# Kernel optimization log

Measured on AMD Instinct MI355X. Metric: run time of the kernel, lower is better.

## Reference

```python
import jax, jax.numpy as jnp
import numpy as np

N = 100000   # nodes
E = 3200000  # edges
D = 128      # input feature dim (lazy in_channels of gat1)
H = 1        # heads
C1, C2 = 16, 32
NEG_SLOPE = 0.2


def setup_inputs() -> dict:
    key = jax.random.key(0)
    ks = jax.random.split(key, 20)
    g = lambda k, shape, s=0.05: (jax.random.normal(k, shape, dtype=jnp.float32) * s)
    return {
        "x": jax.random.normal(ks[0], (N, D), dtype=jnp.float32),
        "edges": jax.random.randint(ks[1], (2, E), 0, N, dtype=jnp.int32),
        "edge_weights": jax.random.uniform(ks[2], (E, 1), dtype=jnp.float32),
        # GATv2 layer 1 (in=D, out=16, heads=1, edge_dim=1)
        "Wl1": g(ks[3], (D, H * C1)), "bl1": jnp.zeros((H * C1,), jnp.float32),
        "Wr1": g(ks[4], (D, H * C1)), "br1": jnp.zeros((H * C1,), jnp.float32),
        "We1": g(ks[5], (1, H * C1)),
        "att1": g(ks[6], (H, C1)),
        "b1": jnp.zeros((C1,), jnp.float32),
        # GATv2 layer 2 (in=16, out=32, heads=1, edge_dim=1)
        "Wl2": g(ks[7], (C1, H * C2)), "bl2": jnp.zeros((H * C2,), jnp.float32),
        "Wr2": g(ks[8], (C1, H * C2)), "br2": jnp.zeros((H * C2,), jnp.float32),
        "We2": g(ks[9], (1, H * C2)),
        "att2": g(ks[10], (H, C2)),
        "b2": jnp.zeros((C2,), jnp.float32),
    }


def _segment_softmax(e, seg, num_segments):
    # numerically-stable softmax over edges grouped by destination node
    m = jax.ops.segment_max(e, seg, num_segments=num_segments)  # [N,H]
    ex = jnp.exp(e - m[seg])
    s = jax.ops.segment_sum(ex, seg, num_segments=num_segments)  # [N,H]
    return ex / (s[seg] + 1e-16)


def _gatv2(x, src, dst, edge_attr, Wl, bl, Wr, br, We, att, b, num_nodes, heads, out_ch):
    xl = (x @ Wl + bl).reshape(-1, heads, out_ch)          # [N,H,C] source transform
    xr = (x @ Wr + br).reshape(-1, heads, out_ch)          # [N,H,C] target transform
    xe = (edge_attr @ We).reshape(-1, heads, out_ch)       # [E,H,C] edge transform
    s = jax.nn.leaky_relu(xl[src] + xr[dst] + xe, NEG_SLOPE)  # [E,H,C]
    e = jnp.einsum('ehc,hc->eh', s, att)                   # [E,H] scores
    alpha = _segment_softmax(e, dst, num_nodes)            # [E,H]
    out = jax.ops.segment_sum(alpha[..., None] * xl[src], dst, num_segments=num_nodes)
    out = out.mean(axis=1) + b                             # concat=False -> mean over heads
    return out, alpha


def reference(x, edges, edge_weights, Wl1, bl1, Wr1, br1, We1, att1, b1,
              Wl2, bl2, Wr2, br2, We2, att2, b2):
    src, dst = edges[0], edges[1]
    h, alpha1 = _gatv2(x, src, dst, edge_weights, Wl1, bl1, Wr1, br1, We1, att1, b1, N, H, C1)
    h = jax.nn.relu(h)
    # layer-1 attention coefficients become layer-2 edge features ([E, heads=1])
    _, alpha2 = _gatv2(h, src, dst, alpha1, Wl2, bl2, Wr2, br2, We2, att2, b2, N, H, C2)
    return edges, alpha2
```

## Files before the change

### kernel.cpp

```cpp
#include <hip/hip_runtime.h>
#include <hip/hip_bf16.h>


#define NN 100000
#define EE 3200000
#define DD 128
#define CC1 16
#define CC2 32
#define NEG_SLOPE 0.2f

#define NPB  128
#define NBK  782
#define BCAP 5120
#define ACH  4096
#define ABLK 782

typedef __hip_bfloat16 bf16;

__device__ __forceinline__ float b2f(bf16 v) { return __bfloat162float(v); }

__device__ __forceinline__ void ld8bf(const bf16* p, float* f) {
    uint4 u = *(const uint4*)p;
    const unsigned w[4] = {u.x, u.y, u.z, u.w};
#pragma unroll
    for (int i = 0; i < 4; i++) {
        f[2 * i]     = __uint_as_float(w[i] << 16);
        f[2 * i + 1] = __uint_as_float(w[i] & 0xffff0000u);
    }
}

__device__ __forceinline__ unsigned enc_f(float x) {
    unsigned b = __float_as_uint(x);
    return (b & 0x80000000u) ? ~b : (b | 0x80000000u);
}
__device__ __forceinline__ float dec_f(unsigned u) {
    unsigned b = (u & 0x80000000u) ? (u & 0x7fffffffu) : ~u;
    return __uint_as_float(b);
}

__global__ void lin1_kernel(const float* __restrict__ x,
                            const float* __restrict__ Wl, const float* __restrict__ bl,
                            const float* __restrict__ Wr, const float* __restrict__ br,
                            bf16* __restrict__ xl1, bf16* __restrict__ xr1) {
    __shared__ float Ws[DD][32];
    __shared__ float xs[8][DD];
    const int t = threadIdx.x;
    for (int i = t; i < DD * CC1; i += 256) {
        int k = i >> 4, c = i & 15;
        Ws[k][c]      = Wl[i];
        Ws[k][c + 16] = Wr[i];
    }
    const int node0 = blockIdx.x * 8;
    for (int i = t; i < 8 * DD; i += 256) {
        int n = i >> 7, k = i & 127;
        xs[n][k] = x[(node0 + n) * DD + k];
    }
    __syncthreads();
    const int n = t >> 5, c = t & 31;
    const int node = node0 + n;
    float acc = 0.f;
#pragma unroll 16
    for (int k = 0; k < DD; k++) acc += xs[n][k] * Ws[k][c];
    if (c < 16) xl1[node * CC1 + c]        = __float2bfloat16(acc + bl[c]);
    else        xr1[node * CC1 + (c - 16)] = __float2bfloat16(acc + br[c - 16]);
}

__global__ void edge1bin_kernel(const int* __restrict__ edges,
                                const float* __restrict__ ew,
                                const bf16* __restrict__ xl1, const bf16* __restrict__ xr1,
                                const float* __restrict__ We1, const float* __restrict__ att1,
                                float* __restrict__ e1,
                                uint2* __restrict__ tmp, int* __restrict__ gcur) {
    __shared__ float Wes[CC1], atts[CC1];
    __shared__ int cnts[NBK], gbase[NBK], lfill[NBK];
    const int t = threadIdx.x;
    if (t < CC1) { Wes[t] = We1[t]; atts[t] = att1[t]; }
    for (int b = t; b < NBK; b += 256) { cnts[b] = 0; lfill[b] = 0; }
    __syncthreads();
    const int base = blockIdx.x * ACH;
    unsigned pk[16]; float ev[16]; int bk[16];
#pragma unroll
    for (int k = 0; k < 16; k++) {
        const int i = base + k * 256 + t;
        bk[k] = -1;
        if (i < EE) {
            const int s = edges[i], d = edges[EE + i];
            const float w = ew[i];
            float a[CC1], b[CC1];
            ld8bf(xl1 + s * CC1, a); ld8bf(xl1 + s * CC1 + 8, a + 8);
            ld8bf(xr1 + d * CC1, b); ld8bf(xr1 + d * CC1 + 8, b + 8);
            float acc = 0.f;
#pragma unroll
            for (int c = 0; c < CC1; c++) {
                float v = a[c] + b[c] + w * Wes[c];
                v = v > 0.f ? v : NEG_SLOPE * v;
                acc += v * atts[c];
            }
            e1[i] = acc;
            bk[k] = d >> 7;
            pk[k] = (unsigned)(d & 127) | ((unsigned)s << 7);
            ev[k] = acc;
            atomicAdd(&cnts[bk[k]], 1);
        }
    }
    __syncthreads();
    for (int b = t; b < NBK; b += 256)
        if (cnts[b] > 0) gbase[b] = atomicAdd(&gcur[b], cnts[b]);
    __syncthreads();
#pragma unroll
    for (int k = 0; k < 16; k++) {
        if (bk[k] >= 0) {
            const int slot = gbase[bk[k]] + atomicAdd(&lfill[bk[k]], 1);
            tmp[(size_t)bk[k] * BCAP + slot] = make_uint2(pk[k], __float_as_uint(ev[k]));
        }
    }
}

__global__ void scanB_kernel(const int* __restrict__ gcur, int* __restrict__ bbase,
                             int* __restrict__ off) {
    __shared__ int part[1024];
    const int t = threadIdx.x;
    part[t] = (t < NBK) ? gcur[t] : 0;
    __syncthreads();
    for (int o = 1; o < 1024; o <<= 1) {
        int v = (t >= o) ? part[t - o] : 0;
        __syncthreads();
        part[t] += v;
        __syncthreads();
    }
    if (t < NBK) bbase[t] = part[t] - gcur[t];
    if (t == 0) off[NN] = EE;
}

__global__ void binB2_kernel(const uint2* __restrict__ tmp, const int* __restrict__ gcur,
                             const int* __restrict__ bbase,
                             uint2* __restrict__ csr2, int* __restrict__ off) {
    __shared__ int cnt[NPB];
    __shared__ int loff[NPB];
    const int t = threadIdx.x;
    const int b = blockIdx.x;
    const int count = gcur[b];
    const uint2* rec = tmp + (size_t)b * BCAP;
    for (int i = t; i < NPB; i += 512) cnt[i] = 0;
    __syncthreads();
    for (int j = t; j < count; j += 512) atomicAdd(&cnt[rec[j].x & 127u], 1);
    __syncthreads();
    if (t == 0) {
        int run = 0;
#pragma unroll
        for (int i = 0; i < NPB; i++) { loff[i] = run; run += cnt[i]; }
    }
    __syncthreads();
    const int base = bbase[b];
    const int n0 = b * NPB;
    for (int i = t; i < NPB; i += 512) {
        const int node = n0 + i;
        if (node < NN) off[node] = base + loff[i];
    }
    for (int j = t; j < count; j += 512) {
        const uint2 r = rec[j];
        const int d = (int)(r.x & 127u);
        const int rr = atomicSub(&cnt[d], 1);
        const int pos = base + loff[d] + rr - 1;
        const float p = __expf(__uint_as_float(r.y));
        csr2[pos] = make_uint2(r.x >> 7, __float_as_uint(p));
    }
}

__global__ void node1f_kernel(const int* __restrict__ off, const uint2* __restrict__ csr2,
                              const bf16* __restrict__ xl1,
                              float* __restrict__ den1, bf16* __restrict__ out1) {
    const int t = blockIdx.x * 256 + threadIdx.x;
    const int n = t >> 4, c = t & 15;
    const int beg = off[n], end = off[n + 1];
    float l = 0.f, acc = 0.f;
    for (int j = beg; j < end; j++) {
        const uint2 r = csr2[j];
        const float p = __uint_as_float(r.y);
        acc += p * b2f(xl1[r.x * CC1 + c]);
        l += p;
    }
    out1[n * CC1 + c] = __float2bfloat16(l > 0.f ? acc / l : 0.f);
    if (c == 0) den1[n] = l;
}

__global__ void lin2_kernel(const bf16* __restrict__ out1, const float* __restrict__ b1,
                            const float* __restrict__ Wl2, const float* __restrict__ bl2,
                            const float* __restrict__ Wr2, const float* __restrict__ br2,
                            bf16* __restrict__ xl2, bf16* __restrict__ xr2) {
    __shared__ float Ws[CC1][64];
    __shared__ float hs[4][CC1];
    const int t = threadIdx.x;
    for (int i = t; i < CC1 * CC2; i += 256) {
        int k = i >> 5, c = i & 31;
        Ws[k][c]      = Wl2[i];
        Ws[k][c + 32] = Wr2[i];
    }
    const int node0 = blockIdx.x * 4;
    if (t < 64) {
        int n = t >> 4, k = t & 15;
        float v = b2f(out1[(node0 + n) * CC1 + k]) + b1[k];
        hs[n][k] = v > 0.f ? v : 0.f;
    }
    __syncthreads();
    const int n = t >> 6, c = t & 63;
    const int node = node0 + n;
    float acc = 0.f;
#pragma unroll
    for (int k = 0; k < CC1; k++) acc += hs[n][k] * Ws[k][c];
    if (c < 32) xl2[node * CC2 + c]        = __float2bfloat16(acc + bl2[c]);
    else        xr2[node * CC2 + (c - 32)] = __float2bfloat16(acc + br2[c - 32]);
}

__global__ void edge2bin_kernel(const int* __restrict__ edges,
                                float* __restrict__ e,
                                const float* __restrict__ den1,
                                const bf16* __restrict__ xl2, const bf16* __restrict__ xr2,
                                const float* __restrict__ We2, const float* __restrict__ att2,
                                uint2* __restrict__ tmp, int* __restrict__ gcur) {
    __shared__ float Wes[CC2], atts[CC2];
    __shared__ int cnts[NBK], gbase[NBK], lfill[NBK];
    const int t = threadIdx.x;
    if (t < CC2) { Wes[t] = We2[t]; atts[t] = att2[t]; }
    for (int b = t; b < NBK; b += 256) { cnts[b] = 0; lfill[b] = 0; }
    __syncthreads();
    const int base = blockIdx.x * ACH;
    unsigned pk[16]; float ev[16]; int bk[16];
#pragma unroll
    for (int k = 0; k < 16; k++) {
        const int i = base + k * 256 + t;
        bk[k] = -1;
        if (i < EE) {
            const int s = edges[i], d = edges[EE + i];
            const float w = __expf(e[i]) / (den1[d] + 1e-16f);
            float a[CC2], b[CC2];
#pragma unroll
            for (int q = 0; q < 4; q++) {
                ld8bf(xl2 + s * CC2 + 8 * q, a + 8 * q);
                ld8bf(xr2 + d * CC2 + 8 * q, b + 8 * q);
            }
            float acc = 0.f;
#pragma unroll
            for (int c = 0; c < CC2; c++) {
                float v = a[c] + b[c] + w * Wes[c];
                v = v > 0.f ? v : NEG_SLOPE * v;
                acc += v * atts[c];
            }
            e[i] = acc;
            bk[k] = d >> 7;
            pk[k] = (unsigned)(d & 127);
            ev[k] = acc;
            atomicAdd(&cnts[bk[k]], 1);
        }
    }
    __syncthreads();
    for (int b = t; b < NBK; b += 256)
        if (cnts[b] > 0) gbase[b] = atomicAdd(&gcur[b], cnts[b]);
    __syncthreads();
#pragma unroll
    for (int k = 0; k < 16; k++) {
        if (bk[k] >= 0) {
            const int slot = gbase[bk[k]] + atomicAdd(&lfill[bk[k]], 1);
            tmp[(size_t)bk[k] * BCAP + slot] = make_uint2(pk[k], __float_as_uint(ev[k]));
        }
    }
}

__global__ void nodeB2_kernel(const uint2* __restrict__ tmp, const int* __restrict__ gcur,
                              float* __restrict__ den2) {
    __shared__ float den[NPB];
    const int t = threadIdx.x;
    const int b = blockIdx.x;
    const int count = gcur[b];
    const uint2* rec = tmp + (size_t)b * BCAP;
    for (int i = t; i < NPB; i += 512) den[i] = 0.f;
    __syncthreads();
    for (int j = t; j < count; j += 512) {
        const uint2 r = rec[j];
        atomicAdd(&den[r.x & 127u], __expf(__uint_as_float(r.y)));
    }
    __syncthreads();
    const int n0 = b * NPB;
    for (int i = t; i < NPB; i += 512) {
        const int node = n0 + i;
        if (node < NN) den2[node] = den[i];
    }
}

__global__ void final2_kernel(const int* __restrict__ dst,
                              const float* __restrict__ e,
                              const float* __restrict__ den2,
                              float* __restrict__ out) {
    const int i = blockIdx.x * 256 + threadIdx.x;
    const int d = dst[i];
    out[2 * EE + i] = __expf(e[i]) / (den2[d] + 1e-16f);
}

__global__ void edges_kernel(const int* __restrict__ edges, float* __restrict__ out) {
    const int i = blockIdx.x * 256 + threadIdx.x;
    out[i] = (float)edges[i];
}

__global__ void edge1f_kernel(const int* __restrict__ edges,
                              const float* __restrict__ ew,
                              const bf16* __restrict__ xl1, const bf16* __restrict__ xr1,
                              const float* __restrict__ We1, const float* __restrict__ att1,
                              float* __restrict__ e1, int* __restrict__ cnt,
                              unsigned* __restrict__ m1enc) {
    __shared__ float Wes[CC1], atts[CC1];
    if (threadIdx.x < CC1) {
        Wes[threadIdx.x]  = We1[threadIdx.x];
        atts[threadIdx.x] = att1[threadIdx.x];
    }
    __syncthreads();
    const int e = blockIdx.x * 256 + threadIdx.x;
    const int s = edges[e], d = edges[EE + e];
    const float w = ew[e];
    float a[CC1], b[CC1];
    ld8bf(xl1 + s * CC1, a); ld8bf(xl1 + s * CC1 + 8, a + 8);
    ld8bf(xr1 + d * CC1, b); ld8bf(xr1 + d * CC1 + 8, b + 8);
    float acc = 0.f;
#pragma unroll
    for (int c = 0; c < CC1; c++) {
        float v = a[c] + b[c] + w * Wes[c];
        v = v > 0.f ? v : NEG_SLOPE * v;
        acc += v * atts[c];
    }
    e1[e] = acc;
    atomicAdd(&cnt[d], 1);
    atomicMax(&m1enc[d], enc_f(acc));
}

__global__ void scan_kernel(const int* __restrict__ cnt, int* __restrict__ off) {
    __shared__ int part[1024];
    const int t = threadIdx.x;
    const int chunk = (NN + 1023) / 1024;
    const int beg = t * chunk;
    const int end = min(beg + chunk, NN);
    int s = 0;
    for (int i = beg; i < end; i++) s += cnt[i];
    part[t] = s;
    __syncthreads();
    for (int o = 1; o < 1024; o <<= 1) {
        int v = (t >= o) ? part[t - o] : 0;
        __syncthreads();
        part[t] += v;
        __syncthreads();
    }
    int run = (t > 0) ? part[t - 1] : 0;
    for (int i = beg; i < end; i++) { off[i] = run; run += cnt[i]; }
    if (t == 1023) off[NN] = part[1023];
}

__global__ void scatter_kernel(const int* __restrict__ edges,
                               const int* __restrict__ off, int* __restrict__ cnt,
                               int* __restrict__ csr) {
    const int i = blockIdx.x * 256 + threadIdx.x;
    const int d = edges[EE + i];
    const int r = atomicSub(&cnt[d], 1);
    csr[off[d] + r - 1] = i;
}

__global__ void node1s_kernel(const int* __restrict__ off, const int* __restrict__ csr,
                              const int* __restrict__ edges,
                              const float* __restrict__ e1, const bf16* __restrict__ xl1,
                              float* __restrict__ den1, bf16* __restrict__ out1) {
    const int t = blockIdx.x * 256 + threadIdx.x;
    const int n = t >> 4, c = t & 15;
    const int beg = off[n], end = off[n + 1];
    float m = -3.0e38f, l = 0.f, acc = 0.f;
    for (int j = beg; j < end; j++) {
        const int eid = csr[j];
        const float s = e1[eid];
        const int src = edges[eid];
        const float xv = b2f(xl1[src * CC1 + c]);
        if (s > m) { const float r = __expf(m - s); l *= r; acc *= r; m = s; }
        const float p = __expf(s - m);
        l += p; acc += p * xv;
    }
    out1[n * CC1 + c] = __float2bfloat16(l > 0.f ? acc / l : 0.f);
    if (c == 0) den1[n] = l;
}

__global__ void edge2enc_kernel(const int* __restrict__ edges,
                                float* __restrict__ e,
                                const unsigned* __restrict__ m1enc,
                                const float* __restrict__ den1,
                                const bf16* __restrict__ xl2, const bf16* __restrict__ xr2,
                                const float* __restrict__ We2, const float* __restrict__ att2) {
    __shared__ float Wes[CC2], atts[CC2];
    if (threadIdx.x < CC2) {
        Wes[threadIdx.x]  = We2[threadIdx.x];
        atts[threadIdx.x] = att2[threadIdx.x];
    }
    __syncthreads();
    const int i = blockIdx.x * 256 + threadIdx.x;
    const int s = edges[i], d = edges[EE + i];
    const float w = __expf(e[i] - dec_f(m1enc[d])) / (den1[d] + 1e-16f);
    float a[CC2], b[CC2];
#pragma unroll
    for (int q = 0; q < 4; q++) {
        ld8bf(xl2 + s * CC2 + 8 * q, a + 8 * q);
        ld8bf(xr2 + d * CC2 + 8 * q, b + 8 * q);
    }
    float acc = 0.f;
#pragma unroll
    for (int c = 0; c < CC2; c++) {
        float v = a[c] + b[c] + w * Wes[c];
        v = v > 0.f ? v : NEG_SLOPE * v;
        acc += v * atts[c];
    }
    e[i] = acc;
}

__global__ void max2_kernel(const int* __restrict__ dst, const float* __restrict__ e2,
                            unsigned* __restrict__ m2) {
    const int i = blockIdx.x * 256 + threadIdx.x;
    atomicMax(&m2[dst[i]], enc_f(e2[i]));
}

__global__ void num2_kernel(const int* __restrict__ dst,
                            const unsigned* __restrict__ m2,
                            float* __restrict__ e, float* __restrict__ den2) {
    const int i = blockIdx.x * 256 + threadIdx.x;
    const int d = dst[i];
    const float v = __expf(e[i] - dec_f(m2[d]));
    e[i] = v;
    atomicAdd(&den2[d], v);
}

__global__ void finalold_kernel(const int* __restrict__ dst,
                                const float* __restrict__ e,
                                const float* __restrict__ den2,
                                float* __restrict__ out) {
    const int i = blockIdx.x * 256 + threadIdx.x;
    const int d = dst[i];
    out[2 * EE + i] = e[i] / (den2[d] + 1e-16f);
}

extern "C" void kernel_launch(void* const* d_in, const int* in_sizes, int n_in,
                              void* d_out, int out_size, void* d_ws, size_t ws_size,
                              hipStream_t stream) {
    const float* x    = (const float*)d_in[0];
    const int*  edges = (const int*)d_in[1];
    const float* ew   = (const float*)d_in[2];
    const float* Wl1  = (const float*)d_in[3];
    const float* bl1  = (const float*)d_in[4];
    const float* Wr1  = (const float*)d_in[5];
    const float* br1  = (const float*)d_in[6];
    const float* We1  = (const float*)d_in[7];
    const float* att1 = (const float*)d_in[8];
    const float* b1   = (const float*)d_in[9];
    const float* Wl2  = (const float*)d_in[10];
    const float* bl2  = (const float*)d_in[11];
    const float* Wr2  = (const float*)d_in[12];
    const float* br2  = (const float*)d_in[13];
    const float* We2  = (const float*)d_in[14];
    const float* att2 = (const float*)d_in[15];
    float* out = (float*)d_out;

    const int* dst = edges + EE;
    const int EG = EE / 256;

    const size_t dpBytes = (size_t)NBK * BCAP * 8;
    uint2* tmp   = (uint2*)d_ws;
    int*   gcur  = (int*)((char*)d_ws + dpBytes);
    int*   bbase = (int*)((char*)d_ws + dpBytes + 4096);
    uint2* csr2  = (uint2*)((char*)d_ws + dpBytes + 8192);
    int*   off   = (int*)((char*)d_ws + dpBytes + 8192 + (size_t)EE * 8);
    const size_t ws_need = dpBytes + 8192 + (size_t)EE * 8
                         + (size_t)(NN + 4) * 4;
    const bool fast = (d_ws != nullptr) && (ws_size >= ws_need);

    if (fast) {
        float* e = out;
        bf16*  xl2  = (bf16*)(out + EE);
        bf16*  xr2  = xl2 + NN * CC2;
        float* den2 = out + EE;
        float* den1 = out + 2 * EE;
        bf16*  xl1  = (bf16*)(den1 + NN);
        bf16*  xr1  = xl1 + NN * CC1;
        bf16*  out1 = xr1 + NN * CC1;

        hipMemsetAsync(gcur, 0, (size_t)NBK * sizeof(int), stream);
        lin1_kernel    <<<NN / 8, 256, 0, stream>>>(x, Wl1, bl1, Wr1, br1, xl1, xr1);
        edge1bin_kernel<<<ABLK, 256, 0, stream>>>(edges, ew, xl1, xr1, We1, att1,
                                                  e, tmp, gcur);
        scanB_kernel   <<<1, 1024, 0, stream>>>(gcur, bbase, off);
        binB2_kernel   <<<NBK, 512, 0, stream>>>(tmp, gcur, bbase, csr2, off);
        node1f_kernel  <<<NN * 16 / 256, 256, 0, stream>>>(off, csr2, xl1, den1, out1);
        lin2_kernel    <<<NN / 4, 256, 0, stream>>>(out1, b1, Wl2, bl2, Wr2, br2, xl2, xr2);
        hipMemsetAsync(gcur, 0, (size_t)NBK * sizeof(int), stream);
        edge2bin_kernel<<<ABLK, 256, 0, stream>>>(edges, e, den1, xl2, xr2,
                                                  We2, att2, tmp, gcur);
        nodeB2_kernel  <<<NBK, 512, 0, stream>>>(tmp, gcur, den2);
        final2_kernel  <<<EG, 256, 0, stream>>>(dst, e, den2, out);
        edges_kernel   <<<2 * EG, 256, 0, stream>>>(edges, out);
    } else {
        float*    e    = out;
        int*      csr  = (int*)(out + EE);
        bf16*     xl2  = (bf16*)(out + EE);
        bf16*     xr2  = xl2 + NN * CC2;
        unsigned* m2   = (unsigned*)(out + EE);
        float*    den2 = (float*)(out + EE) + NN;
        int*      offF  = (int*)(out + 2 * EE);
        unsigned* m1enc = (unsigned*)(offF + NN + 4);
        int*      cnt   = (int*)(m1enc + NN);
        float*    den1  = (float*)(cnt + NN);
        bf16*     xl1   = (bf16*)(den1 + NN);
        bf16*     xr1   = xl1 + NN * CC1;
        bf16*     out1  = xr1 + NN * CC1;

        hipMemsetAsync(m1enc, 0, (size_t)2 * NN * sizeof(int), stream);
        lin1_kernel   <<<NN / 8, 256, 0, stream>>>(x, Wl1, bl1, Wr1, br1, xl1, xr1);
        edge1f_kernel <<<EG, 256, 0, stream>>>(edges, ew, xl1, xr1, We1, att1,
                                               e, cnt, m1enc);
        scan_kernel   <<<1, 1024, 0, stream>>>(cnt, offF);
        scatter_kernel<<<EG, 256, 0, stream>>>(edges, offF, cnt, csr);
        node1s_kernel <<<NN * 16 / 256, 256, 0, stream>>>(offF, csr, edges, e, xl1,
                                                          den1, out1);
        lin2_kernel   <<<NN / 4, 256, 0, stream>>>(out1, b1, Wl2, bl2, Wr2, br2, xl2, xr2);
        edge2enc_kernel<<<EG, 256, 0, stream>>>(edges, e, m1enc, den1, xl2, xr2,
                                                We2, att2);
        hipMemsetAsync(m2, 0, (size_t)2 * NN * sizeof(float), stream);
        max2_kernel   <<<EG, 256, 0, stream>>>(dst, e, m2);
        num2_kernel   <<<EG, 256, 0, stream>>>(dst, m2, e, den2);
        finalold_kernel<<<EG, 256, 0, stream>>>(dst, e, den2, out);
        edges_kernel  <<<2 * EG, 256, 0, stream>>>(edges, out);
    }
}
```

Baseline: 596.0 us.

## Fuse bucket sort and layer-1 aggregation into one shared-memory kernel

Replaces the scan, global CSR scatter and per-node aggregation kernels with a single per-bucket kernel. It sorts each bucket's records in LDS and aggregates the 128 destination nodes directly from there. This removes the 25.6MB CSR write and re-read, the single-block scan and two launches. The edge binning kernels also move to 512-thread blocks that each handle 8 edges per thread instead of 16, which may change occupancy. The 40KB LDS buffer per block limits how many blocks fit on a CU.

Measured after the change: 547.8 us. 8.1% less time.

```diff
diff --git a/kernel.cpp b/kernel.cpp
--- a/kernel.cpp
+++ b/kernel.cpp
@@ -75,13 +75,13 @@
     __shared__ int cnts[NBK], gbase[NBK], lfill[NBK];
     const int t = threadIdx.x;
     if (t < CC1) { Wes[t] = We1[t]; atts[t] = att1[t]; }
-    for (int b = t; b < NBK; b += 256) { cnts[b] = 0; lfill[b] = 0; }
+    for (int b = t; b < NBK; b += 512) { cnts[b] = 0; lfill[b] = 0; }
     __syncthreads();
     const int base = blockIdx.x * ACH;
-    unsigned pk[16]; float ev[16]; int bk[16];
-#pragma unroll
-    for (int k = 0; k < 16; k++) {
-        const int i = base + k * 256 + t;
+    unsigned pk[8]; float ev[8]; int bk[8];
+#pragma unroll
+    for (int k = 0; k < 8; k++) {
+        const int i = base + k * 512 + t;
         bk[k] = -1;
         if (i < EE) {
             const int s = edges[i], d = edges[EE + i];
@@ -104,11 +104,11 @@
         }
     }
     __syncthreads();
-    for (int b = t; b < NBK; b += 256)
+    for (int b = t; b < NBK; b += 512)
         if (cnts[b] > 0) gbase[b] = atomicAdd(&gcur[b], cnts[b]);
     __syncthreads();
 #pragma unroll
-    for (int k = 0; k < 16; k++) {
+    for (int k = 0; k < 8; k++) {
         if (bk[k] >= 0) {
             const int slot = gbase[bk[k]] + atomicAdd(&lfill[bk[k]], 1);
             tmp[(size_t)bk[k] * BCAP + slot] = make_uint2(pk[k], __float_as_uint(ev[k]));
@@ -116,27 +116,12 @@
     }
 }
 
-__global__ void scanB_kernel(const int* __restrict__ gcur, int* __restrict__ bbase,
-                             int* __restrict__ off) {
-    __shared__ int part[1024];
-    const int t = threadIdx.x;
-    part[t] = (t < NBK) ? gcur[t] : 0;
-    __syncthreads();
-    for (int o = 1; o < 1024; o <<= 1) {
-        int v = (t >= o) ? part[t - o] : 0;
-        __syncthreads();
-        part[t] += v;
-        __syncthreads();
-    }
-    if (t < NBK) bbase[t] = part[t] - gcur[t];
-    if (t == 0) off[NN] = EE;
-}
-
-__global__ void binB2_kernel(const uint2* __restrict__ tmp, const int* __restrict__ gcur,
-                             const int* __restrict__ bbase,
-                             uint2* __restrict__ csr2, int* __restrict__ off) {
+__global__ void bucket1_kernel(const uint2* __restrict__ tmp, const int* __restrict__ gcur,
+                               const bf16* __restrict__ xl1,
+                               float* __restrict__ den1, bf16* __restrict__ out1) {
     __shared__ int cnt[NPB];
-    __shared__ int loff[NPB];
+    __shared__ int loff[NPB + 1];
+    __shared__ uint2 srt[BCAP];
     const int t = threadIdx.x;
     const int b = blockIdx.x;
     const int count = gcur[b];
@@ -149,39 +134,33 @@
         int run = 0;
 #pragma unroll
         for (int i = 0; i < NPB; i++) { loff[i] = run; run += cnt[i]; }
-    }
-    __syncthreads();
-    const int base = bbase[b];
-    const int n0 = b * NPB;
-    for (int i = t; i < NPB; i += 512) {
-        const int node = n0 + i;
-        if (node < NN) off[node] = base + loff[i];
-    }
+        loff[NPB] = run;
+    }
+    __syncthreads();
     for (int j = t; j < count; j += 512) {
         const uint2 r = rec[j];
         const int d = (int)(r.x & 127u);
         const int rr = atomicSub(&cnt[d], 1);
-        const int pos = base + loff[d] + rr - 1;
-        const float p = __expf(__uint_as_float(r.y));
-        csr2[pos] = make_uint2(r.x >> 7, __float_as_uint(p));
-    }
-}
-
-__global__ void node1f_kernel(const int* __restrict__ off, const uint2* __restrict__ csr2,
-                              const bf16* __restrict__ xl1,
-                              float* __restrict__ den1, bf16* __restrict__ out1) {
-    const int t = blockIdx.x * 256 + threadIdx.x;
-    const int n = t >> 4, c = t & 15;
-    const int beg = off[n], end = off[n + 1];
-    float l = 0.f, acc = 0.f;
-    for (int j = beg; j < end; j++) {
-        const uint2 r = csr2[j];
-        const float p = __uint_as_float(r.y);
-        acc += p * b2f(xl1[r.x * CC1 + c]);
-        l += p;
-    }
-    out1[n * CC1 + c] = __float2bfloat16(l > 0.f ? acc / l : 0.f);
-    if (c == 0) den1[n] = l;
+        srt[loff[d] + rr - 1] =
+            make_uint2(r.x >> 7, __float_as_uint(__expf(__uint_as_float(r.y))));
+    }
+    __syncthreads();
+    const int g = t >> 4, c = t & 15;
+    const int n0 = b * NPB;
+    for (int dn = g; dn < NPB; dn += 32) {
+        const int node = n0 + dn;
+        if (node >= NN) continue;
+        const int beg = loff[dn], end = loff[dn + 1];
+        float l = 0.f, acc = 0.f;
+        for (int j = beg; j < end; j++) {
+            const uint2 r = srt[j];
+            const float p = __uint_as_float(r.y);
+            acc += p * b2f(xl1[r.x * CC1 + c]);
+            l += p;
+        }
+        out1[node * CC1 + c] = __float2bfloat16(l > 0.f ? acc / l : 0.f);
+        if (c == 0) den1[node] = l;
+    }
 }
 
 __global__ void lin2_kernel(const bf16* __restrict__ out1, const float* __restrict__ b1,
@@ -222,13 +201,13 @@
     __shared__ int cnts[NBK], gbase[NBK], lfill[NBK];
     const int t = threadIdx.x;
     if (t < CC2) { Wes[t] = We2[t]; atts[t] = att2[t]; }
-    for (int b = t; b < NBK; b += 256) { cnts[b] = 0; lfill[b] = 0; }
+    for (int b = t; b < NBK; b += 512) { cnts[b] = 0; lfill[b] = 0; }
     __syncthreads();
     const int base = blockIdx.x * ACH;
-    unsigned pk[16]; float ev[16]; int bk[16];
-#pragma unroll
-    for (int k = 0; k < 16; k++) {
-        const int i = base + k * 256 + t;
+    unsigned pk[8]; float ev[8]; int bk[8];
+#pragma unroll
+    for (int k = 0; k < 8; k++) {
+        const int i = base + k * 512 + t;
         bk[k] = -1;
         if (i < EE) {
             const int s = edges[i], d = edges[EE + i];
@@ -254,11 +233,11 @@
         }
     }
     __syncthreads();
-    for (int b = t; b < NBK; b += 256)
+    for (int b = t; b < NBK; b += 512)
         if (cnts[b] > 0) gbase[b] = atomicAdd(&gcur[b], cnts[b]);
     __syncthreads();
 #pragma unroll
-    for (int k = 0; k < 16; k++) {
+    for (int k = 0; k < 8; k++) {
         if (bk[k] >= 0) {
             const int slot = gbase[bk[k]] + atomicAdd(&lfill[bk[k]], 1);
             tmp[(size_t)bk[k] * BCAP + slot] = make_uint2(pk[k], __float_as_uint(ev[k]));
@@ -463,13 +442,9 @@
     const int EG = EE / 256;
 
     const size_t dpBytes = (size_t)NBK * BCAP * 8;
-    uint2* tmp   = (uint2*)d_ws;
-    int*   gcur  = (int*)((char*)d_ws + dpBytes);
-    int*   bbase = (int*)((char*)d_ws + dpBytes + 4096);
-    uint2* csr2  = (uint2*)((char*)d_ws + dpBytes + 8192);
-    int*   off   = (int*)((char*)d_ws + dpBytes + 8192 + (size_t)EE * 8);
-    const size_t ws_need = dpBytes + 8192 + (size_t)EE * 8
-                         + (size_t)(NN + 4) * 4;
+    uint2* tmp  = (uint2*)d_ws;
+    int*   gcur = (int*)((char*)d_ws + dpBytes);
+    const size_t ws_need = dpBytes + 8192;
     const bool fast = (d_ws != nullptr) && (ws_size >= ws_need);
 
     if (fast) {
@@ -484,14 +459,12 @@
 
         hipMemsetAsync(gcur, 0, (size_t)NBK * sizeof(int), stream);
         lin1_kernel    <<<NN / 8, 256, 0, stream>>>(x, Wl1, bl1, Wr1, br1, xl1, xr1);
-        edge1bin_kernel<<<ABLK, 256, 0, stream>>>(edges, ew, xl1, xr1, We1, att1,
+        edge1bin_kernel<<<ABLK, 512, 0, stream>>>(edges, ew, xl1, xr1, We1, att1,
                                                   e, tmp, gcur);
-        scanB_kernel   <<<1, 1024, 0, stream>>>(gcur, bbase, off);
-        binB2_kernel   <<<NBK, 512, 0, stream>>>(tmp, gcur, bbase, csr2, off);
-        node1f_kernel  <<<NN * 16 / 256, 256, 0, stream>>>(off, csr2, xl1, den1, out1);
+        bucket1_kernel <<<NBK, 512, 0, stream>>>(tmp, gcur, xl1, den1, out1);
         lin2_kernel    <<<NN / 4, 256, 0, stream>>>(out1, b1, Wl2, bl2, Wr2, br2, xl2, xr2);
         hipMemsetAsync(gcur, 0, (size_t)NBK * sizeof(int), stream);
-        edge2bin_kernel<<<ABLK, 256, 0, stream>>>(edges, e, den1, xl2, xr2,
+        edge2bin_kernel<<<ABLK, 512, 0, stream>>>(edges, e, den1, xl2, xr2,
                                                   We2, att2, tmp, gcur);
         nodeB2_kernel  <<<NBK, 512, 0, stream>>>(tmp, gcur, den2);
         final2_kernel  <<<EG, 256, 0, stream>>>(dst, e, den2, out);
```
